# Kernel optimization log

Measured on AMD Instinct MI355X. Metric: run time of the kernel, lower is better.

## Reference

```python
import jax, jax.numpy as jnp
import numpy as np

V = 4
H, W, Z = 32, 64, 13
C = 256
NH = 8
WS = (4, 4, 1)
SS = (2, 2, 0)
HID = 1024


def _layernorm(x, g, b):
    mu = jnp.mean(x, axis=-1, keepdims=True)
    var = jnp.mean((x - mu) ** 2, axis=-1, keepdims=True)
    return (x - mu) * jax.lax.rsqrt(var + 1e-5) * g + b


def setup_inputs() -> dict:
    key = jax.random.key(0)
    ks = jax.random.split(key, 12)
    B = 2
    s = 0.02
    return {
        "x_z": jax.random.normal(ks[0], (B, H, W, Z, C), jnp.float32),
        "x_q": jax.random.normal(ks[1], (B, H, W, Z, C), jnp.float32),
        "x_t": jax.random.normal(ks[2], (B, H, W, Z, C), jnp.float32),
        "x_u": jax.random.normal(ks[3], (B, H, W, Z, C), jnp.float32),
        "qkv_w": jax.random.normal(ks[4], (V, C, 3 * C), jnp.float32) * s,
        "qkv_b": jnp.zeros((V, 3 * C), jnp.float32),
        "proj_w": jax.random.normal(ks[5], (V, C, C), jnp.float32) * s,
        "proj_b": jnp.zeros((V, C), jnp.float32),
        "n1_g": jnp.ones((V, C), jnp.float32),
        "n1_b": jnp.zeros((V, C), jnp.float32),
        "n2_g": jnp.ones((V, C), jnp.float32),
        "n2_b": jnp.zeros((V, C), jnp.float32),
        "fc1_w": jax.random.normal(ks[6], (V, C, HID), jnp.float32) * s,
        "fc1_b": jnp.zeros((V, HID), jnp.float32),
        "fc2_w": jax.random.normal(ks[7], (V, HID, C), jnp.float32) * s,
        "fc2_b": jnp.zeros((V, C), jnp.float32),
    }


def reference(x_z, x_q, x_t, x_u, qkv_w, qkv_b, proj_w, proj_b,
              n1_g, n1_b, n2_g, n2_b, fc1_w, fc1_b, fc2_w, fc2_b):
    x = jnp.stack([x_z, x_q, x_t, x_u], axis=0)  # [V,B,H,W,Z,C]
    B = x.shape[1]
    L = H * W * Z
    w0, w1, w2 = WS
    N = w0 * w1 * w2
    hd = C // NH
    scale = hd ** -0.5

    shortcut = x.reshape(V, B, L, C)
    xn = _layernorm(shortcut, n1_g[:, None, None, :], n1_b[:, None, None, :])
    xs = xn.reshape(V, B, H, W, Z, C)
    # cyclic shift (same sign used for both rolls in the source)
    xs = jnp.roll(xs, shift=SS, axis=(2, 3, 4))
    # window partition -> [V, B_, N, C]
    xw = xs.reshape(V, B, H // w0, w0, W // w1, w1, Z // w2, w2, C)
    xw = xw.transpose(0, 1, 2, 4, 6, 3, 5, 7, 8).reshape(V, -1, N, C)
    B_ = xw.shape[1]

    qkv = jnp.einsum('vbnc,vcd->vbnd', xw, qkv_w) + qkv_b[:, None, None, :]
    qkv = qkv.reshape(V, B_, N, 3, NH, hd).transpose(3, 1, 0, 4, 2, 5)  # [3,B_,V,NH,N,hd]
    q, k, v = qkv[0], qkv[1], qkv[2]
    # per-(variable, head) attention: heads of different variables are concatenated
    attn = jax.nn.softmax(jnp.einsum('bvhnd,bvhmd->bvhnm', q * scale, k), axis=-1)
    ctx = jnp.einsum('bvhnm,bvhmd->bvhnd', attn, v)  # [B_,V,NH,N,hd]
    # faithful to torch reshape (B_, N, V*NH, hd) -> (B_, V*N, C): rows interleave (n, v)
    big = ctx.transpose(0, 3, 1, 2, 4).reshape(B_, V * N, C)
    y = big.reshape(B_, V, N, C).transpose(1, 0, 2, 3)  # slice [:, i*N:(i+1)*N]
    y = jnp.einsum('vbnc,vcd->vbnd', y, proj_w) + proj_b[:, None, None, :]
    # window reverse
    y = y.reshape(V, B, H // w0, W // w1, Z // w2, w0, w1, w2, C)
    y = y.transpose(0, 1, 2, 5, 3, 6, 4, 7, 8).reshape(V, B, H, W, Z, C)
    y = jnp.roll(y, shift=SS, axis=(2, 3, 4))  # same-sign roll (preserves source behavior)
    y = y.reshape(V, B, L, C)

    x2 = shortcut + y
    xm = _layernorm(x2, n2_g[:, None, None, :], n2_b[:, None, None, :])
    h = jax.nn.gelu(jnp.einsum('vblc,vcd->vbld', xm, fc1_w) + fc1_b[:, None, None, :],
                    approximate=False)
    m = jnp.einsum('vbld,vdc->vblc', h, fc2_w) + fc2_b[:, None, None, :]
    out = (x2 + m).reshape(V, B, H, W, Z, C)
    return out  # stacked per-variable outputs in variable_order
```

## Files before the change

kernel.cpp:

```cpp
#include <hip/hip_runtime.h>
#include <hip/hip_bf16.h>
#include <cstdint>
#include <cstddef>

#define DI __device__ __forceinline__

typedef __bf16 bf16_t;
typedef bf16_t bf16x8 __attribute__((ext_vector_type(8)));
typedef float f32x4 __attribute__((ext_vector_type(4)));

constexpr int Vn = 4, Bn = 2, Hn = 32, Wn = 64, Zn = 13, Cn = 256, HIDn = 1024;
constexpr int Ln = Hn * Wn * Zn;
constexpr int BWn = Bn * (Hn / 4) * (Wn / 4) * Zn;
constexpr int PB = Bn * Ln;
constexpr int ROWS = Vn * PB;

DI void gload_lds16(const void* g, void* l) {
  __builtin_amdgcn_global_load_lds(
      (const __attribute__((address_space(1))) void*)g,
      (__attribute__((address_space(3))) void*)l, 16, 0, 0);
}

DI unsigned short f2bf_bits(float f) {
  __hip_bfloat16 h = __float2bfloat16(f);
  return *reinterpret_cast<unsigned short*>(&h);
}

DI float gelu_f(float x) {
  float u = x * x;
  float w = x * fmaf(0.044715f, u, 1.0f);
  float e = __expf(-1.5957691216057308f * w);
  return x * __builtin_amdgcn_rcpf(1.0f + e);
}

__global__ __launch_bounds__(256) void transpose_tile_kernel(
    const float* __restrict__ src, __hip_bfloat16* __restrict__ dst, int K, int N) {
  __shared__ float S[64][65];
  const int n0 = blockIdx.x * 64, k0 = blockIdx.y * 64, v = blockIdx.z;
  const int tc = threadIdx.x & 63, tr = threadIdx.x >> 6;
#pragma unroll
  for (int i = 0; i < 16; ++i) {
    int kk = tr + i * 4;
    S[kk][tc] = src[((size_t)v * K + k0 + kk) * N + n0 + tc];
  }
  __syncthreads();
#pragma unroll
  for (int i = 0; i < 16; ++i) {
    int nn = tr + i * 4;
    dst[((size_t)v * N + n0 + nn) * K + k0 + tc] = __float2bfloat16(S[tc][nn]);
  }
}

__global__ __launch_bounds__(256) void ln1_kernel(
    const float* __restrict__ x0, const float* __restrict__ x1,
    const float* __restrict__ x2i, const float* __restrict__ x3,
    const float* __restrict__ g_, const float* __restrict__ b_,
    __hip_bfloat16* __restrict__ xw) {
  int gw = blockIdx.x * 4 + (threadIdx.x >> 6);
  int lane = threadIdx.x & 63;
  int v = gw / PB;
  int rem = gw - v * PB;
  int bw = rem >> 4, nn = rem & 15;
  int zb = bw % 13;
  int t = bw / 13;
  int wb = t & 15, t2 = t >> 4;
  int hb = t2 & 7, b = t2 >> 3;
  int hs = (hb * 4 + (nn >> 2) + 30) & 31;
  int wsrc = (wb * 4 + (nn & 3) + 62) & 63;
  size_t l = (size_t)(hs * 64 + wsrc) * 13 + zb;
  const float* xv = (v == 0) ? x0 : (v == 1) ? x1 : (v == 2) ? x2i : x3;
  const float* xp = xv + ((size_t)b * Ln + l) * 256;
  float4 val = *(const float4*)(xp + lane * 4);
  float s = val.x + val.y + val.z + val.w;
  float sq = val.x * val.x + val.y * val.y + val.z * val.z + val.w * val.w;
#pragma unroll
  for (int o = 32; o; o >>= 1) {
    s += __shfl_xor(s, o);
    sq += __shfl_xor(sq, o);
  }
  float mean = s * (1.0f / 256.0f);
  float var = sq * (1.0f / 256.0f) - mean * mean;
  float rstd = rsqrtf(var + 1e-5f);
  const float* gg = g_ + v * 256 + lane * 4;
  const float* bb = b_ + v * 256 + lane * 4;
  ushort4 o4;
  o4.x = f2bf_bits((val.x - mean) * rstd * gg[0] + bb[0]);
  o4.y = f2bf_bits((val.y - mean) * rstd * gg[1] + bb[1]);
  o4.z = f2bf_bits((val.z - mean) * rstd * gg[2] + bb[2]);
  o4.w = f2bf_bits((val.w - mean) * rstd * gg[3] + bb[3]);
  *reinterpret_cast<ushort4*>(xw + (size_t)gw * 256 + lane * 4) = o4;
}

__global__ __launch_bounds__(256) void attn_kernel(
    const __hip_bfloat16* __restrict__ qkvp, __hip_bfloat16* __restrict__ ctx) {
  __shared__ float P[4][16][17];
  int b_ = blockIdx.x;
  int v = blockIdx.y;
  int wid = threadIdx.x >> 6, lane = threadIdx.x & 63;
  int lm = lane & 15, hi = lane >> 4;
  const bf16_t* base = (const bf16_t*)qkvp + (size_t)(v * BWn + b_) * 16 * 768;
  const float scale = 0.17677669529663687f;
  f32x4 zero = {0.f, 0.f, 0.f, 0.f};
#pragma unroll
  for (int hh = 0; hh < 2; ++hh) {
    int h = wid + 4 * hh;
    bf16x8 qf = *(const bf16x8*)(base + (size_t)lm * 768 + h * 32 + hi * 8);
    bf16x8 kf = *(const bf16x8*)(base + (size_t)lm * 768 + 256 + h * 32 + hi * 8);
    f32x4 s = __builtin_amdgcn_mfma_f32_16x16x32_bf16(qf, kf, zero, 0, 0, 0);
    float p0[4];
#pragma unroll
    for (int q = 0; q < 4; ++q) {
      float val = s[q] * scale;
      float mx = val;
#pragma unroll
      for (int o = 8; o >= 1; o >>= 1) mx = fmaxf(mx, __shfl_xor(mx, o));
      float e = __expf(val - mx);
      float sum = e;
#pragma unroll
      for (int o = 8; o >= 1; o >>= 1) sum += __shfl_xor(sum, o);
      p0[q] = e * __builtin_amdgcn_rcpf(sum);
    }
#pragma unroll
    for (int q = 0; q < 4; ++q) P[wid][hi * 4 + q][lm] = p0[q];
    bf16x8 pa;
#pragma unroll
    for (int j = 0; j < 8; ++j) pa[j] = (bf16_t)0.f;
    if (hi < 2) {
#pragma unroll
      for (int j = 0; j < 8; ++j) pa[j] = (bf16_t)P[wid][lm][hi * 8 + j];
    }
#pragma unroll
    for (int dh = 0; dh < 2; ++dh) {
      bf16x8 vf;
#pragma unroll
      for (int j = 0; j < 8; ++j) vf[j] = (bf16_t)0.f;
      if (hi < 2) {
#pragma unroll
        for (int j = 0; j < 8; ++j)
          vf[j] = base[(size_t)(hi * 8 + j) * 768 + 512 + h * 32 + dh * 16 + lm];
      }
      f32x4 c = __builtin_amdgcn_mfma_f32_16x16x32_bf16(pa, vf, zero, 0, 0, 0);
#pragma unroll
      for (int q = 0; q < 4; ++q) {
        int n = hi * 4 + q;
        int d = dh * 16 + lm;
        int r = n * 4 + v;
        int vo = r >> 4, no = r & 15;
        ctx[((size_t)(vo * BWn + b_) * 16 + no) * 256 + h * 32 + d] = __float2bfloat16(c[q]);
      }
    }
  }
}

template <int EPI, int K, int N>
__global__ __launch_bounds__(256, 3) void gemm4(
    const __hip_bfloat16* __restrict__ A, const __hip_bfloat16* __restrict__ WT,
    const float* __restrict__ bias, __hip_bfloat16* __restrict__ outb,
    float* __restrict__ outf, const float* __restrict__ xi0,
    const float* __restrict__ xi1, const float* __restrict__ xi2,
    const float* __restrict__ xi3) {
  constexpr int NT = K / 64;
  constexpr int NC = N / 128;
  const int v = blockIdx.z;
  const int x = blockIdx.x;
  const int xcd = x & 7;
  const int j = x >> 3;
  const int c = j % NC;
  const int r = xcd + 8 * (j / NC);
  const int rowBase = r * 128;
  const int colBase = c * 128;

  const bf16_t* Av = (const bf16_t*)A + ((size_t)v * PB + rowBase) * K;
  const bf16_t* Wv = (const bf16_t*)WT + ((size_t)v * N + colBase) * K;

  __shared__ __align__(16) uint8_t smem[40960];
  bf16_t(*As)[64] = (bf16_t(*)[64])smem;
  bf16_t(*Bs)[64] = (bf16_t(*)[64])(smem + 16384);

  const int tid = threadIdx.x, wid = tid >> 6, lane = tid & 63;
  const int wr = wid >> 1, wc = wid & 1;
  const int lm = lane & 15, hi = lane >> 4;
  const int rA = lane >> 3;
  const int lg = (lane & 7) ^ rA;

  f32x4 acc[4][4];
#pragma unroll
  for (int m = 0; m < 4; ++m)
#pragma unroll
    for (int n = 0; n < 4; ++n) acc[m][n] = f32x4{0.f, 0.f, 0.f, 0.f};

  for (int t = 0; t < NT; ++t) {
    if (t) __syncthreads();
#pragma unroll
    for (int g = 0; g < 4; ++g) {
      int grp = wid * 4 + g;
      gload_lds16(Av + (size_t)(grp * 8 + rA) * K + t * 64 + lg * 8, &As[grp * 8][0]);
    }
#pragma unroll
    for (int g = 0; g < 4; ++g) {
      int grp = wid * 4 + g;
      gload_lds16(Wv + (size_t)(grp * 8 + rA) * K + t * 64 + lg * 8, &Bs[grp * 8][0]);
    }
    __syncthreads();
#pragma unroll
    for (int kk = 0; kk < 2; ++kk) {
      bf16x8 af[4], bfv[4];
#pragma unroll
      for (int m = 0; m < 4; ++m) {
        const int rr = wr * 64 + m * 16 + lm;
        af[m] = *(const bf16x8*)&As[rr][((kk * 4 + hi) ^ (lm & 7)) * 8];
      }
#pragma unroll
      for (int n = 0; n < 4; ++n) {
        const int rr = wc * 64 + n * 16 + lm;
        bfv[n] = *(const bf16x8*)&Bs[rr][((kk * 4 + hi) ^ (lm & 7)) * 8];
      }
#pragma unroll
      for (int m = 0; m < 4; ++m)
#pragma unroll
        for (int n = 0; n < 4; ++n)
          acc[m][n] = __builtin_amdgcn_mfma_f32_16x16x32_bf16(af[m], bfv[n], acc[m][n], 0, 0, 0);
    }
  }

  __syncthreads();
  uint8_t* ep = smem + wid * 10240;

  if constexpr (EPI == 0) {
    ushort(*E)[72] = (ushort(*)[72])ep;
    float bcol[4];
#pragma unroll
    for (int n = 0; n < 4; ++n) bcol[n] = bias[v * N + colBase + wc * 64 + n * 16 + lm];
#pragma unroll
    for (int m = 0; m < 4; ++m)
#pragma unroll
      for (int q = 0; q < 4; ++q) {
        int lr = m * 16 + hi * 4 + q;
#pragma unroll
        for (int n = 0; n < 4; ++n) E[lr][n * 16 + lm] = f2bf_bits(acc[m][n][q] + bcol[n]);
      }
    const int pr = lane >> 3, pc = lane & 7;
#pragma unroll
    for (int p = 0; p < 8; ++p) {
      int lr = p * 8 + pr;
      bf16x8 val = *(const bf16x8*)&E[lr][pc * 8];
      size_t grow = (size_t)v * PB + rowBase + wr * 64 + lr;
      int gcol = colBase + wc * 64 + pc * 8;
      *(bf16x8*)&outb[grow * N + gcol] = val;
    }
  } else {
    float(*F)[36] = (float(*)[36])ep;
    const int pr = lane >> 3, pc = lane & 7;
#pragma unroll
    for (int h2 = 0; h2 < 2; ++h2) {
#pragma unroll
      for (int m = 0; m < 4; ++m)
#pragma unroll
        for (int q = 0; q < 4; ++q) {
          int lr = m * 16 + hi * 4 + q;
#pragma unroll
          for (int n2 = 0; n2 < 2; ++n2) F[lr][n2 * 16 + lm] = acc[m][h2 * 2 + n2][q];
        }
#pragma unroll
      for (int p = 0; p < 8; ++p) {
        int lr = p * 8 + pr;
        f32x4 a4 = *(const f32x4*)&F[lr][pc * 4];
        int rowv = rowBase + wr * 64 + lr;
        int gcol = colBase + wc * 64 + h2 * 32 + pc * 4;
        f32x4 b4 = *(const f32x4*)&bias[v * N + gcol];
        int b_ = rowv >> 4, nn = rowv & 15;
        int zb = b_ % 13;
        int tt = b_ / 13;
        int wb = tt & 15, tt2 = tt >> 4;
        int hb = tt2 & 7, bb = tt2 >> 3;
        int h2v = (hb * 4 + (nn >> 2) + 2) & 31;
        int w2v = (wb * 4 + (nn & 3) + 2) & 63;
        size_t l = (size_t)(h2v * 64 + w2v) * 13 + zb;
        const float* xv = (v == 0) ? xi0 : (v == 1) ? xi1 : (v == 2) ? xi2 : xi3;
        f32x4 x4 = *(const f32x4*)(xv + ((size_t)bb * Ln + l) * 256 + gcol);
        f32x4 o4 = a4 + b4 + x4;
        *(f32x4*)(outf + (((size_t)v * Bn + bb) * Ln + l) * 256 + gcol) = o4;
      }
      if (h2 == 0) __builtin_amdgcn_s_waitcnt(0);
    }
  }
}

__global__ __launch_bounds__(512, 4) void mlp_fused8(
    const float* __restrict__ x2,
    const __hip_bfloat16* __restrict__ W1T,
    const __hip_bfloat16* __restrict__ W2T,
    const float* __restrict__ b1, const float* __restrict__ b2,
    const float* __restrict__ g2, const float* __restrict__ bt2,
    float* __restrict__ outp) {
  const int v = blockIdx.z;
  const size_t gRow0 = (size_t)v * PB + (size_t)blockIdx.x * 64;

  __shared__ __align__(16) uint8_t smem[69632];
  uint8_t* hb = smem + 65536;

  const int tid = threadIdx.x, wid = tid >> 6, lane = tid & 63;
  const int lm = lane & 15, hi = lane >> 4;
  const int wa = wid >> 2, wb = wid & 3;
  const int rA = lane >> 3, lg = (lane & 7) ^ rA;

  {
    f32x4 g4 = *(const f32x4*)(g2 + v * 256 + lane * 4);
    f32x4 b4l = *(const f32x4*)(bt2 + v * 256 + lane * 4);
    for (int i = 0; i < 8; ++i) {
      int r = wid * 8 + i;
      const float* xp = x2 + (gRow0 + r) * 256;
      float4 val = *(const float4*)(xp + lane * 4);
      float s = val.x + val.y + val.z + val.w;
      float sq = val.x * val.x + val.y * val.y + val.z * val.z + val.w * val.w;
#pragma unroll
      for (int o = 32; o; o >>= 1) {
        s += __shfl_xor(s, o);
        sq += __shfl_xor(sq, o);
      }
      float mean = s * (1.0f / 256.0f);
      float var = sq * (1.0f / 256.0f) - mean * mean;
      float rstd = rsqrtf(var + 1e-5f);
      ushort4 o4;
      o4.x = f2bf_bits((val.x - mean) * rstd * g4[0] + b4l[0]);
      o4.y = f2bf_bits((val.y - mean) * rstd * g4[1] + b4l[1]);
      o4.z = f2bf_bits((val.z - mean) * rstd * g4[2] + b4l[2]);
      o4.w = f2bf_bits((val.w - mean) * rstd * g4[3] + b4l[3]);
      int gph = ((lm >> 1) ^ (r & 7) ^ hi) & 7;
      *(ushort4*)(smem + hi * 8192 + r * 128 + gph * 16 + (lm & 1) * 8) = o4;
    }
  }
  __syncthreads();

  bf16x8 xnf[4][2];
  {
    int r = wb * 16 + lm;
#pragma unroll
    for (int t = 0; t < 4; ++t)
#pragma unroll
      for (int kk = 0; kk < 2; ++kk) {
        int gph = ((kk * 4 + hi) ^ (r & 7) ^ t) & 7;
        xnf[t][kk] = *(const bf16x8*)(smem + t * 8192 + r * 128 + gph * 16);
      }
  }

  int off_w1[8];
  {
    int hw = wa * 16 + lm;
#pragma unroll
    for (int t = 0; t < 4; ++t)
#pragma unroll
      for (int kk = 0; kk < 2; ++kk)
        off_w1[t * 2 + kk] = t * 4096 + hw * 128 + (((kk * 4 + hi) ^ (hw & 7)) & 7) * 16;
  }
  int off_w2[8];
#pragma unroll
  for (int ca = 0; ca < 8; ++ca) {
    int col = wa * 128 + ca * 16 + lm;
    int p2 = col >> 1;
    off_w2[ca] = p2 * 128 + ((((col & 1) * 4 + hi) ^ (p2 & 7)) & 7) * 16;
  }
  int off_hf, off_hw;
  {
    int xr = wb * 16 + lm;
    int p = xr >> 1;
    off_hf = p * 128 + ((((xr & 1) * 4 + hi) ^ (p & 7)) & 7) * 16;
    int glog = (xr & 1) * 4 + wa * 2 + (hi >> 1);
    off_hw = p * 128 + ((glog ^ (p & 7)) & 7) * 16 + (hi & 1) * 8;
  }
  int gsrc_w1[2], ldst_w1[2], gsrc_w2[2], ldst_w2[2];
#pragma unroll
  for (int s = 0; s < 2; ++s) {
    int idx = wid * 2 + s;
    int t = idx >> 2, grp = idx & 3;
    gsrc_w1[s] = (grp * 8 + rA) * 256 + t * 64 + lg * 8;
    ldst_w1[s] = t * 4096 + grp * 1024;
    int i = wid * 2 + s;
    int p = i * 8 + rA;
    int col = 2 * p + (lg >> 2);
    gsrc_w2[s] = col * 1024 + (lg & 3) * 8;
    ldst_w2[s] = i * 1024;
  }

  f32x4 acc2[8];
#pragma unroll
  for (int ca = 0; ca < 8; ++ca) acc2[ca] = f32x4{0.f, 0.f, 0.f, 0.f};

  const bf16_t* W1v = (const bf16_t*)W1T + (size_t)v * 1024 * 256;
  const bf16_t* W2v = (const bf16_t*)W2T + (size_t)v * 256 * 1024;

  auto stageW = [&](uint8_t* W1c, uint8_t* W2c, int hc) {
#pragma unroll
    for (int s = 0; s < 2; ++s)
      gload_lds16(W1v + (size_t)hc * 32 * 256 + gsrc_w1[s], W1c + ldst_w1[s]);
#pragma unroll
    for (int s = 0; s < 2; ++s)
      gload_lds16(W2v + hc * 32 + gsrc_w2[s], W2c + ldst_w2[s]);
  };

  auto chunk = [&](uint8_t* W1c, uint8_t* W2c, uint8_t* W1n, uint8_t* W2n,
                   int hc, bool stage_next) {
    if (stage_next) stageW(W1n, W2n, hc + 1);
    f32x4 acc1 = f32x4{0.f, 0.f, 0.f, 0.f};
#pragma unroll
    for (int j = 0; j < 8; ++j) {
      bf16x8 w1f = *(const bf16x8*)(W1c + off_w1[j]);
      acc1 = __builtin_amdgcn_mfma_f32_16x16x32_bf16(w1f, xnf[j >> 1][j & 1], acc1, 0, 0, 0);
    }
    {
      f32x4 b1v = *(const f32x4*)&b1[v * 1024 + hc * 32 + wa * 16 + hi * 4];
      ushort4 hp;
      hp.x = f2bf_bits(gelu_f(acc1[0] + b1v[0]));
      hp.y = f2bf_bits(gelu_f(acc1[1] + b1v[1]));
      hp.z = f2bf_bits(gelu_f(acc1[2] + b1v[2]));
      hp.w = f2bf_bits(gelu_f(acc1[3] + b1v[3]));
      *(ushort4*)(hb + off_hw) = hp;
    }
    __syncthreads();
    {
      bf16x8 hf = *(const bf16x8*)(hb + off_hf);
#pragma unroll
      for (int ca = 0; ca < 8; ++ca) {
        bf16x8 w2f = *(const bf16x8*)(W2c + off_w2[ca]);
        acc2[ca] = __builtin_amdgcn_mfma_f32_16x16x32_bf16(w2f, hf, acc2[ca], 0, 0, 0);
      }
    }
    __syncthreads();
  };

  stageW(smem + 32768, smem + 49152, 0);
  __syncthreads();

#pragma unroll 1
  for (int i = 0; i < 16; ++i) {
    chunk(smem + 32768, smem + 49152, smem, smem + 16384, 2 * i, true);
    chunk(smem, smem + 16384, smem + 32768, smem + 49152, 2 * i + 1, i != 15);
  }

  {
    size_t orow = gRow0 + wb * 16 + lm;
    float* obase = outp + orow * 256;
#pragma unroll
    for (int ca = 0; ca < 8; ++ca) {
      int col = wa * 128 + ca * 16 + hi * 4;
      f32x4 b4 = *(const f32x4*)&b2[v * 256 + col];
      float* o = obase + col;
      f32x4 cur = *(const f32x4*)o;
      f32x4 res = cur + acc2[ca] + b4;
      *(f32x4*)o = res;
    }
  }
}

extern "C" void kernel_launch(void* const* d_in, const int* in_sizes, int n_in,
                              void* d_out, int out_size, void* d_ws, size_t ws_size,
                              hipStream_t stream) {
  const float* x0 = (const float*)d_in[0];
  const float* x1 = (const float*)d_in[1];
  const float* x2i = (const float*)d_in[2];
  const float* x3 = (const float*)d_in[3];
  const float* qkv_w = (const float*)d_in[4];
  const float* qkv_b = (const float*)d_in[5];
  const float* proj_w = (const float*)d_in[6];
  const float* proj_b = (const float*)d_in[7];
  const float* n1g = (const float*)d_in[8];
  const float* n1b = (const float*)d_in[9];
  const float* n2g = (const float*)d_in[10];
  const float* n2b = (const float*)d_in[11];
  const float* fc1_w = (const float*)d_in[12];
  const float* fc1_b = (const float*)d_in[13];
  const float* fc2_w = (const float*)d_in[14];
  const float* fc2_b = (const float*)d_in[15];
  float* out = (float*)d_out;

  uint8_t* ws = (uint8_t*)d_ws;
  size_t off = 0;
  auto alloc = [&](size_t bytes) -> void* {
    void* p = ws + off;
    off += (bytes + 255) & ~(size_t)255;
    return p;
  };
  __hip_bfloat16* wqkvT = (__hip_bfloat16*)alloc((size_t)Vn * Cn * 768 * 2);
  __hip_bfloat16* wprojT = (__hip_bfloat16*)alloc((size_t)Vn * Cn * Cn * 2);
  __hip_bfloat16* wfc1T = (__hip_bfloat16*)alloc((size_t)Vn * Cn * HIDn * 2);
  __hip_bfloat16* wfc2T = (__hip_bfloat16*)alloc((size_t)Vn * HIDn * Cn * 2);
  __hip_bfloat16* xw = (__hip_bfloat16*)alloc((size_t)ROWS * Cn * 2);
  __hip_bfloat16* qkvb = (__hip_bfloat16*)alloc((size_t)ROWS * 768 * 2);

  transpose_tile_kernel<<<dim3(768 / 64, 256 / 64, Vn), 256, 0, stream>>>(qkv_w, wqkvT, 256, 768);
  transpose_tile_kernel<<<dim3(256 / 64, 256 / 64, Vn), 256, 0, stream>>>(proj_w, wprojT, 256, 256);
  transpose_tile_kernel<<<dim3(1024 / 64, 256 / 64, Vn), 256, 0, stream>>>(fc1_w, wfc1T, 256, 1024);
  transpose_tile_kernel<<<dim3(256 / 64, 1024 / 64, Vn), 256, 0, stream>>>(fc2_w, wfc2T, 1024, 256);

  ln1_kernel<<<ROWS / 4, 256, 0, stream>>>(x0, x1, x2i, x3, n1g, n1b, xw);

  gemm4<0, 256, 768><<<dim3(416 * 6, 1, Vn), 256, 0, stream>>>(
      xw, wqkvT, qkv_b, qkvb, nullptr, nullptr, nullptr, nullptr, nullptr);

  attn_kernel<<<dim3(BWn, Vn), 256, 0, stream>>>(qkvb, xw );

  gemm4<1, 256, 256><<<dim3(416 * 2, 1, Vn), 256, 0, stream>>>(
      xw , wprojT, proj_b, nullptr, out , x0, x1, x2i, x3);

  mlp_fused8<<<dim3(PB / 64, 1, Vn), 512, 0, stream>>>(
      out , wfc1T, wfc2T, fc1_b, fc2_b, n2g, n2b, out);
}
```

Before: 853.0 us.

## Software-pipeline fused MLP: overlap GEMM1 of next chunk with GEMM2 of previous

Restructures the fused MLP inner loop so that each iteration computes fc1+GELU for hidden chunk i while running the fc2 accumulation for chunk i-1, using a double-buffered hidden-activation tile. This halves the number of block-wide barriers per chunk (one instead of two) and staggers W1 and W2 staging so more MFMA work is independent between syncs. LDS use grows by 4 KB, which may affect occupancy at 4 blocks per CU of 512 threads.

```diff
diff --git a/kernel.cpp b/kernel.cpp
--- a/kernel.cpp
+++ b/kernel.cpp
@@ -286,7 +286,7 @@
   }
 }
 
-__global__ __launch_bounds__(512, 4) void mlp_fused8(
+__global__ __launch_bounds__(512, 4) void mlp_fused10(
     const float* __restrict__ x2,
     const __hip_bfloat16* __restrict__ W1T,
     const __hip_bfloat16* __restrict__ W2T,
@@ -296,8 +296,13 @@
   const int v = blockIdx.z;
   const size_t gRow0 = (size_t)v * PB + (size_t)blockIdx.x * 64;
 
-  __shared__ __align__(16) uint8_t smem[69632];
-  uint8_t* hb = smem + 65536;
+  __shared__ __align__(16) uint8_t smem[73728];
+  uint8_t* w1b0 = smem + 32768;
+  uint8_t* w2b0 = smem + 49152;
+  uint8_t* w1b1 = smem;
+  uint8_t* w2b1 = smem + 16384;
+  uint8_t* hb0 = smem + 65536;
+  uint8_t* hb1 = smem + 69632;
 
   const int tid = threadIdx.x, wid = tid >> 6, lane = tid & 63;
   const int lm = lane & 15, hi = lane >> 4;
@@ -389,53 +394,71 @@
   const bf16_t* W1v = (const bf16_t*)W1T + (size_t)v * 1024 * 256;
   const bf16_t* W2v = (const bf16_t*)W2T + (size_t)v * 256 * 1024;
 
-  auto stageW = [&](uint8_t* W1c, uint8_t* W2c, int hc) {
+  auto stageW1 = [&](uint8_t* dst, int hc) {
 #pragma unroll
     for (int s = 0; s < 2; ++s)
-      gload_lds16(W1v + (size_t)hc * 32 * 256 + gsrc_w1[s], W1c + ldst_w1[s]);
+      gload_lds16(W1v + (size_t)hc * 32 * 256 + gsrc_w1[s], dst + ldst_w1[s]);
+  };
+  auto stageW2 = [&](uint8_t* dst, int hc) {
 #pragma unroll
     for (int s = 0; s < 2; ++s)
-      gload_lds16(W2v + hc * 32 + gsrc_w2[s], W2c + ldst_w2[s]);
+      gload_lds16(W2v + hc * 32 + gsrc_w2[s], dst + ldst_w2[s]);
   };
 
-  auto chunk = [&](uint8_t* W1c, uint8_t* W2c, uint8_t* W1n, uint8_t* W2n,
-                   int hc, bool stage_next) {
-    if (stage_next) stageW(W1n, W2n, hc + 1);
+  auto gemm1 = [&](uint8_t* w1_rd, uint8_t* h_wr, int hc) {
     f32x4 acc1 = f32x4{0.f, 0.f, 0.f, 0.f};
 #pragma unroll
     for (int j = 0; j < 8; ++j) {
-      bf16x8 w1f = *(const bf16x8*)(W1c + off_w1[j]);
+      bf16x8 w1f = *(const bf16x8*)(w1_rd + off_w1[j]);
       acc1 = __builtin_amdgcn_mfma_f32_16x16x32_bf16(w1f, xnf[j >> 1][j & 1], acc1, 0, 0, 0);
     }
-    {
-      f32x4 b1v = *(const f32x4*)&b1[v * 1024 + hc * 32 + wa * 16 + hi * 4];
-      ushort4 hp;
-      hp.x = f2bf_bits(gelu_f(acc1[0] + b1v[0]));
-      hp.y = f2bf_bits(gelu_f(acc1[1] + b1v[1]));
-      hp.z = f2bf_bits(gelu_f(acc1[2] + b1v[2]));
-      hp.w = f2bf_bits(gelu_f(acc1[3] + b1v[3]));
-      *(ushort4*)(hb + off_hw) = hp;
-    }
+    f32x4 b1v = *(const f32x4*)&b1[v * 1024 + hc * 32 + wa * 16 + hi * 4];
+    ushort4 hp;
+    hp.x = f2bf_bits(gelu_f(acc1[0] + b1v[0]));
+    hp.y = f2bf_bits(gelu_f(acc1[1] + b1v[1]));
+    hp.z = f2bf_bits(gelu_f(acc1[2] + b1v[2]));
+    hp.w = f2bf_bits(gelu_f(acc1[3] + b1v[3]));
+    *(ushort4*)(h_wr + off_hw) = hp;
+  };
+
+  auto gemm2 = [&](uint8_t* w2_rd, uint8_t* h_rd) {
+    bf16x8 hf = *(const bf16x8*)(h_rd + off_hf);
+#pragma unroll
+    for (int ca = 0; ca < 8; ++ca) {
+      bf16x8 w2f = *(const bf16x8*)(w2_rd + off_w2[ca]);
+      acc2[ca] = __builtin_amdgcn_mfma_f32_16x16x32_bf16(w2f, hf, acc2[ca], 0, 0, 0);
+    }
+  };
+
+  stageW1(w1b0, 0);
+  __syncthreads();
+
+  stageW1(w1b1, 1);
+  stageW2(w2b0, 0);
+  gemm1(w1b0, hb0, 0);
+  __syncthreads();
+
+#pragma unroll 1
+  for (int j = 0; j < 15; ++j) {
+    const int i = 2 * j + 1;
+    stageW1(w1b0, i + 1);
+    stageW2(w2b1, i);
+    gemm1(w1b1, hb1, i);
+    gemm2(w2b0, hb0);
     __syncthreads();
-    {
-      bf16x8 hf = *(const bf16x8*)(hb + off_hf);
-#pragma unroll
-      for (int ca = 0; ca < 8; ++ca) {
-        bf16x8 w2f = *(const bf16x8*)(W2c + off_w2[ca]);
-        acc2[ca] = __builtin_amdgcn_mfma_f32_16x16x32_bf16(w2f, hf, acc2[ca], 0, 0, 0);
-      }
-    }
+    stageW1(w1b1, i + 2);
+    stageW2(w2b0, i + 1);
+    gemm1(w1b0, hb0, i + 1);
+    gemm2(w2b1, hb1);
     __syncthreads();
-  };
-
-  stageW(smem + 32768, smem + 49152, 0);
+  }
+
+  stageW2(w2b1, 31);
+  gemm1(w1b1, hb1, 31);
+  gemm2(w2b0, hb0);
   __syncthreads();
 
-#pragma unroll 1
-  for (int i = 0; i < 16; ++i) {
-    chunk(smem + 32768, smem + 49152, smem, smem + 16384, 2 * i, true);
-    chunk(smem, smem + 16384, smem + 32768, smem + 49152, 2 * i + 1, i != 15);
-  }
+  gemm2(w2b1, hb1);
 
   {
     size_t orow = gRow0 + wb * 16 + lm;
@@ -502,6 +525,6 @@
   gemm4<1, 256, 256><<<dim3(416 * 2, 1, Vn), 256, 0, stream>>>(
       xw , wprojT, proj_b, nullptr, out , x0, x1, x2i, x3);
 
-  mlp_fused8<<<dim3(PB / 64, 1, Vn), 512, 0, stream>>>(
+  mlp_fused10<<<dim3(PB / 64, 1, Vn), 512, 0, stream>>>(
       out , wfc1T, wfc2T, fc1_b, fc2_b, n2g, n2b, out);
 }
```

Result: no change. 853.0 us (-0.0%).

## Fuse LayerNorm1 into QKV GEMM with LDS-resident normalized A tile

Applied to the files above, without the earlier changes.

Replaces the separate LN1 kernel and QKV GEMM with one kernel. Each block normalizes 128 shifted-window rows straight into swizzled LDS, then streams weight tiles to compute a 128x128 QKV output tile. This removes the bf16 xw round trip through global memory and one launch. In exchange, LN is recomputed for each of the 6 column tiles, so fp32 input reads rise about sixfold. The 80KB LDS footprint may also limit occupancy.

```diff
diff --git a/kernel.cpp b/kernel.cpp
--- a/kernel.cpp
+++ b/kernel.cpp
@@ -51,44 +51,132 @@
   }
 }
 
-__global__ __launch_bounds__(256) void ln1_kernel(
+__global__ __launch_bounds__(512, 2) void qkv_ln_kernel(
     const float* __restrict__ x0, const float* __restrict__ x1,
     const float* __restrict__ x2i, const float* __restrict__ x3,
     const float* __restrict__ g_, const float* __restrict__ b_,
-    __hip_bfloat16* __restrict__ xw) {
-  int gw = blockIdx.x * 4 + (threadIdx.x >> 6);
-  int lane = threadIdx.x & 63;
-  int v = gw / PB;
-  int rem = gw - v * PB;
-  int bw = rem >> 4, nn = rem & 15;
-  int zb = bw % 13;
-  int t = bw / 13;
-  int wb = t & 15, t2 = t >> 4;
-  int hb = t2 & 7, b = t2 >> 3;
-  int hs = (hb * 4 + (nn >> 2) + 30) & 31;
-  int wsrc = (wb * 4 + (nn & 3) + 62) & 63;
-  size_t l = (size_t)(hs * 64 + wsrc) * 13 + zb;
+    const __hip_bfloat16* __restrict__ WT,
+    const float* __restrict__ bias,
+    __hip_bfloat16* __restrict__ outb) {
+  constexpr int K = 256, N = 768, NC = 6;
+  const int v = blockIdx.z;
+  const int x = blockIdx.x;
+  const int xcd = x & 7;
+  const int j = x >> 3;
+  const int c = j % NC;
+  const int r = xcd + 8 * (j / NC);
+  const int rowBase = r * 128;
+  const int colBase = c * 128;
+
+  __shared__ __align__(16) uint8_t smem[81920];
+  uint8_t* Bs = smem + 65536;
+
+  const int tid = threadIdx.x, wid = tid >> 6, lane = tid & 63;
+  const int wr = wid >> 1, wc = wid & 1;
+  const int lm = lane & 15, hi = lane >> 4;
+  const int rA = lane >> 3, lg = (lane & 7) ^ rA;
+
   const float* xv = (v == 0) ? x0 : (v == 1) ? x1 : (v == 2) ? x2i : x3;
-  const float* xp = xv + ((size_t)b * Ln + l) * 256;
-  float4 val = *(const float4*)(xp + lane * 4);
-  float s = val.x + val.y + val.z + val.w;
-  float sq = val.x * val.x + val.y * val.y + val.z * val.z + val.w * val.w;
-#pragma unroll
-  for (int o = 32; o; o >>= 1) {
-    s += __shfl_xor(s, o);
-    sq += __shfl_xor(sq, o);
-  }
-  float mean = s * (1.0f / 256.0f);
-  float var = sq * (1.0f / 256.0f) - mean * mean;
-  float rstd = rsqrtf(var + 1e-5f);
-  const float* gg = g_ + v * 256 + lane * 4;
-  const float* bb = b_ + v * 256 + lane * 4;
-  ushort4 o4;
-  o4.x = f2bf_bits((val.x - mean) * rstd * gg[0] + bb[0]);
-  o4.y = f2bf_bits((val.y - mean) * rstd * gg[1] + bb[1]);
-  o4.z = f2bf_bits((val.z - mean) * rstd * gg[2] + bb[2]);
-  o4.w = f2bf_bits((val.w - mean) * rstd * gg[3] + bb[3]);
-  *reinterpret_cast<ushort4*>(xw + (size_t)gw * 256 + lane * 4) = o4;
+
+  {
+    f32x4 g4 = *(const f32x4*)(g_ + v * 256 + lane * 4);
+    f32x4 b4l = *(const f32x4*)(b_ + v * 256 + lane * 4);
+    for (int i = 0; i < 16; ++i) {
+      int row = wid * 16 + i;
+      int rem = rowBase + row;
+      int bw = rem >> 4, nn = rem & 15;
+      int zb = bw % 13;
+      int t = bw / 13;
+      int wb = t & 15, t2 = t >> 4;
+      int hb = t2 & 7, b = t2 >> 3;
+      int hs = (hb * 4 + (nn >> 2) + 30) & 31;
+      int wsrc = (wb * 4 + (nn & 3) + 62) & 63;
+      size_t l = (size_t)(hs * 64 + wsrc) * 13 + zb;
+      const float* xp = xv + ((size_t)b * Ln + l) * 256;
+      float4 val = *(const float4*)(xp + lane * 4);
+      float s = val.x + val.y + val.z + val.w;
+      float sq = val.x * val.x + val.y * val.y + val.z * val.z + val.w * val.w;
+#pragma unroll
+      for (int o = 32; o; o >>= 1) {
+        s += __shfl_xor(s, o);
+        sq += __shfl_xor(sq, o);
+      }
+      float mean = s * (1.0f / 256.0f);
+      float var = sq * (1.0f / 256.0f) - mean * mean;
+      float rstd = rsqrtf(var + 1e-5f);
+      ushort4 o4;
+      o4.x = f2bf_bits((val.x - mean) * rstd * g4[0] + b4l[0]);
+      o4.y = f2bf_bits((val.y - mean) * rstd * g4[1] + b4l[1]);
+      o4.z = f2bf_bits((val.z - mean) * rstd * g4[2] + b4l[2]);
+      o4.w = f2bf_bits((val.w - mean) * rstd * g4[3] + b4l[3]);
+      int gph = ((lm >> 1) ^ (row & 7) ^ hi) & 7;
+      *(ushort4*)(smem + hi * 16384 + row * 128 + gph * 16 + (lm & 1) * 8) = o4;
+    }
+  }
+  __syncthreads();
+
+  const bf16_t* Wv = (const bf16_t*)WT + ((size_t)v * N + colBase) * K;
+
+  f32x4 acc[2][4];
+#pragma unroll
+  for (int m = 0; m < 2; ++m)
+#pragma unroll
+    for (int n = 0; n < 4; ++n) acc[m][n] = f32x4{0.f, 0.f, 0.f, 0.f};
+
+  for (int t = 0; t < 4; ++t) {
+    if (t) __syncthreads();
+#pragma unroll
+    for (int g = 0; g < 2; ++g) {
+      int grp = wid * 2 + g;
+      gload_lds16(Wv + (size_t)(grp * 8 + rA) * K + t * 64 + lg * 8, Bs + grp * 8 * 128);
+    }
+    __syncthreads();
+#pragma unroll
+    for (int kk = 0; kk < 2; ++kk) {
+      bf16x8 af[2], bfv[4];
+#pragma unroll
+      for (int m = 0; m < 2; ++m) {
+        int rr = wr * 32 + m * 16 + lm;
+        int gph = ((kk * 4 + hi) ^ (lm & 7) ^ t) & 7;
+        af[m] = *(const bf16x8*)(smem + t * 16384 + rr * 128 + gph * 16);
+      }
+#pragma unroll
+      for (int n = 0; n < 4; ++n) {
+        int rr = wc * 64 + n * 16 + lm;
+        bfv[n] = *(const bf16x8*)(Bs + rr * 128 + (((kk * 4 + hi) ^ (lm & 7)) & 7) * 16);
+      }
+#pragma unroll
+      for (int m = 0; m < 2; ++m)
+#pragma unroll
+        for (int n = 0; n < 4; ++n)
+          acc[m][n] = __builtin_amdgcn_mfma_f32_16x16x32_bf16(af[m], bfv[n], acc[m][n], 0, 0, 0);
+    }
+  }
+  __syncthreads();
+
+  {
+    ushort(*E)[72] = (ushort(*)[72])(smem + wid * 8192);
+    float bcol[4];
+#pragma unroll
+    for (int n = 0; n < 4; ++n) bcol[n] = bias[v * N + colBase + wc * 64 + n * 16 + lm];
+#pragma unroll
+    for (int m = 0; m < 2; ++m)
+#pragma unroll
+      for (int q = 0; q < 4; ++q) {
+        int lr = m * 16 + hi * 4 + q;
+#pragma unroll
+        for (int n = 0; n < 4; ++n) E[lr][n * 16 + lm] = f2bf_bits(acc[m][n][q] + bcol[n]);
+      }
+    const int pr = lane >> 3, pc = lane & 7;
+#pragma unroll
+    for (int p = 0; p < 4; ++p) {
+      int lr = p * 8 + pr;
+      bf16x8 val = *(const bf16x8*)&E[lr][pc * 8];
+      size_t grow = (size_t)v * PB + rowBase + wr * 32 + lr;
+      int gcol = colBase + wc * 64 + pc * 8;
+      *(bf16x8*)&outb[grow * N + gcol] = val;
+    }
+  }
 }
 
 __global__ __launch_bounds__(256) void attn_kernel(
@@ -226,29 +314,7 @@
   __syncthreads();
   uint8_t* ep = smem + wid * 10240;
 
-  if constexpr (EPI == 0) {
-    ushort(*E)[72] = (ushort(*)[72])ep;
-    float bcol[4];
-#pragma unroll
-    for (int n = 0; n < 4; ++n) bcol[n] = bias[v * N + colBase + wc * 64 + n * 16 + lm];
-#pragma unroll
-    for (int m = 0; m < 4; ++m)
-#pragma unroll
-      for (int q = 0; q < 4; ++q) {
-        int lr = m * 16 + hi * 4 + q;
-#pragma unroll
-        for (int n = 0; n < 4; ++n) E[lr][n * 16 + lm] = f2bf_bits(acc[m][n][q] + bcol[n]);
-      }
-    const int pr = lane >> 3, pc = lane & 7;
-#pragma unroll
-    for (int p = 0; p < 8; ++p) {
-      int lr = p * 8 + pr;
-      bf16x8 val = *(const bf16x8*)&E[lr][pc * 8];
-      size_t grow = (size_t)v * PB + rowBase + wr * 64 + lr;
-      int gcol = colBase + wc * 64 + pc * 8;
-      *(bf16x8*)&outb[grow * N + gcol] = val;
-    }
-  } else {
+  {
     float(*F)[36] = (float(*)[36])ep;
     const int pr = lane >> 3, pc = lane & 7;
 #pragma unroll
@@ -492,10 +558,8 @@
   transpose_tile_kernel<<<dim3(1024 / 64, 256 / 64, Vn), 256, 0, stream>>>(fc1_w, wfc1T, 256, 1024);
   transpose_tile_kernel<<<dim3(256 / 64, 1024 / 64, Vn), 256, 0, stream>>>(fc2_w, wfc2T, 1024, 256);
 
-  ln1_kernel<<<ROWS / 4, 256, 0, stream>>>(x0, x1, x2i, x3, n1g, n1b, xw);
-
-  gemm4<0, 256, 768><<<dim3(416 * 6, 1, Vn), 256, 0, stream>>>(
-      xw, wqkvT, qkv_b, qkvb, nullptr, nullptr, nullptr, nullptr, nullptr);
+  qkv_ln_kernel<<<dim3((PB / 128) * 6, 1, Vn), 512, 0, stream>>>(
+      x0, x1, x2i, x3, n1g, n1b, wqkvT, qkv_b, qkvb);
 
   attn_kernel<<<dim3(BWn, Vn), 256, 0, stream>>>(qkvb, xw );
 
```

New measurement: 1.045 ms. 22.5% more time.
